# Kernel optimization log

Measured on AMD Instinct MI355X. Metric: run time of the kernel, lower is better.

## Reference

```python
import jax, jax.numpy as jnp
import numpy as np

B, N_UNK, M_KNOWN = 8, 8192, 2048
C1, C2 = 256, 256
MLP = [512, 256, 256]
K_ENC = 32
D = MLP[-1]


def setup_inputs() -> dict:
    key = jax.random.key(0)
    ks = jax.random.split(key, 16)
    return {
        "unknown": jax.random.normal(ks[0], (B, N_UNK, 3), jnp.float32),
        "known": jax.random.normal(ks[1], (B, M_KNOWN, 3), jnp.float32),
        "unknow_feats": jax.random.normal(ks[2], (B, C1, N_UNK), jnp.float32),
        "known_feats": jax.random.normal(ks[3], (B, C2, M_KNOWN), jnp.float32),
        "conv_w1": jax.random.normal(ks[4], (MLP[1], MLP[0]), jnp.float32) * 0.05,
        "conv_b1": jnp.zeros((MLP[1],), jnp.float32),
        "bn_g1": jnp.ones((MLP[1],), jnp.float32),
        "bn_b1": jnp.zeros((MLP[1],), jnp.float32),
        "bn_m1": jax.random.normal(ks[5], (MLP[1],), jnp.float32) * 0.01,
        "bn_v1": jax.random.uniform(ks[6], (MLP[1],), jnp.float32, 0.5, 1.5),
        "conv_w2": jax.random.normal(ks[7], (MLP[2], MLP[1]), jnp.float32) * 0.05,
        "conv_b2": jnp.zeros((MLP[2],), jnp.float32),
        "bn_g2": jnp.ones((MLP[2],), jnp.float32),
        "bn_b2": jnp.zeros((MLP[2],), jnp.float32),
        "bn_m2": jax.random.normal(ks[8], (MLP[2],), jnp.float32) * 0.01,
        "bn_v2": jax.random.uniform(ks[9], (MLP[2],), jnp.float32, 0.5, 1.5),
        "enc_codewords": jax.random.normal(ks[10], (K_ENC, D), jnp.float32) * float(1.0 / np.sqrt(K_ENC * D)),
        "enc_scale": jax.random.uniform(ks[11], (K_ENC,), jnp.float32, -1.0, 0.0),
        "lin_w": jax.random.normal(ks[12], (D, D * K_ENC), jnp.float32) * 0.02,
        "lin_b": jnp.zeros((D,), jnp.float32),
    }


def _conv_bn_relu(x, w, b, g, beta, mean, var):
    # 1x1 conv over (B,C,N) == channel GEMM, then BN (inference form), then ReLU
    x = jnp.einsum("oc,bcn->bon", w, x) + b[None, :, None]
    x = g[None, :, None] * (x - mean[None, :, None]) * jax.lax.rsqrt(var + 1e-5)[None, :, None] + beta[None, :, None]
    return jax.nn.relu(x)


def reference(unknown, known, unknow_feats, known_feats,
              conv_w1, conv_b1, bn_g1, bn_b1, bn_m1, bn_v1,
              conv_w2, conv_b2, bn_g2, bn_b2, bn_m2, bn_v2,
              enc_codewords, enc_scale, lin_w, lin_b):
    # ---- three_nn: 3 nearest known points for each unknown point ----
    x2 = jnp.sum(unknown * unknown, axis=-1)            # (B,n)
    y2 = jnp.sum(known * known, axis=-1)                # (B,m)
    d2 = x2[:, :, None] - 2.0 * jnp.einsum("bnc,bmc->bnm", unknown, known) + y2[:, None, :]
    dist = jnp.sqrt(jnp.maximum(d2, 1e-12))             # (B,n,m) Euclidean
    neg_d, idx = jax.lax.top_k(-dist, 3)                # 3 smallest
    dist3 = -neg_d                                      # (B,n,3)
    dist_recip = 1.0 / (dist3 + 1e-8)
    weight = dist_recip / jnp.sum(dist_recip, axis=2, keepdims=True)
    # ---- three_interpolate: gather + weighted sum ----
    gathered = jax.vmap(lambda f, i: f[:, i])(known_feats, idx)   # (B,C2,n,3)
    interp = jnp.einsum("bcnk,bnk->bcn", gathered, weight)        # (B,C2,n)
    feats = jnp.concatenate([interp, unknow_feats], axis=1)       # (B,C2+C1,n)
    # ---- SharedMLP (two 1x1 conv + BN + ReLU layers) ----
    h = _conv_bn_relu(feats, conv_w1, conv_b1, bn_g1, bn_b1, bn_m1, bn_v1)
    h = _conv_bn_relu(h, conv_w2, conv_b2, bn_g2, bn_b2, bn_m2, bn_v2)   # (B,D,n)
    # ---- Encoding layer (soft dictionary assignment, residual aggregate) ----
    X = jnp.swapaxes(h, 1, 2)                                     # (B,n,D)
    c2 = jnp.sum(enc_codewords * enc_codewords, axis=-1)          # (K,)
    xn2 = jnp.sum(X * X, axis=-1)                                 # (B,n)
    # scaled_l2: s_k * ||x - c_k||^2 without materializing (B,n,K,D) residuals
    sl = enc_scale[None, None, :] * (xn2[:, :, None] - 2.0 * jnp.einsum("bnd,kd->bnk", X, enc_codewords) + c2[None, None, :])
    A = jax.nn.softmax(sl, axis=-1)                               # (B,n,K)
    E = jnp.einsum("bnk,bnd->bkd", A, X) - jnp.sum(A, axis=1)[:, :, None] * enc_codewords[None]
    E = jax.nn.relu(E).reshape(E.shape[0], -1)                    # (B,K*D)
    E = E / jnp.maximum(jnp.linalg.norm(E, axis=1, keepdims=True), 1e-12)  # F.normalize
    ctx = jax.nn.sigmoid(E @ lin_w.T + lin_b)                     # (B,D)
    # ---- channel-attention fusion ----
    return h * ctx[:, :, None]                                    # (B,D,n)
```

## Files before the change

kernel.cpp:

```cpp
#include <hip/hip_runtime.h>
#include <stdint.h>

typedef unsigned short u16;
typedef unsigned int u32;
typedef __attribute__((ext_vector_type(8))) short short8;
typedef __attribute__((ext_vector_type(4))) float f32x4;
typedef __attribute__((ext_vector_type(4))) u32 u32x4;

#define B_ 8
#define N_ 8192
#define M_ 2048
#define DD 256
#define KENC 32

#define SC1 0
#define SH1 256
#define SC2 512
#define SH2 768
#define C2OFF 1024
#define SOFF 1056
#define RNOFF 1088

#define OFF_IDX3   0ull
#define OFF_W3     786432ull
#define OFF_FT     1572864ull
#define OFF_H1T    68681728ull
#define OFF_ERELU  102236160ull
#define OFF_PART   102498304ull
#define OFF_CONSTS 102760448ull
#define OFF_CTX    102768640ull
#define OFF_W1D    102776832ull
#define OFF_W2D    103038976ull
#define OFF_CWD    103170048ull
#define OFF_FLAG   103186432ull

__device__ __forceinline__ float bf2f(u16 v){ return __uint_as_float(((u32)v)<<16); }
__device__ __forceinline__ u16 f2bf(float f){
  u32 x = __float_as_uint(f);
  return (u16)((x + 0x7FFFu + ((x>>16)&1u)) >> 16);
}
__device__ __forceinline__ float ldf(const void* p, size_t i, int f){
  return f ? ((const float*)p)[i] : bf2f(((const u16*)p)[i]);
}

__global__ __launch_bounds__(256) void k_detect(const void* v1, int* flagp){
  __shared__ int cntb, cntf;
  int t = threadIdx.x;
  if (t==0){ cntb=0; cntf=0; }
  __syncthreads();
  float vb = bf2f(((const u16*)v1)[t]);
  if (!(vb > 0.4f && vb < 1.6f)) atomicAdd(&cntb, 1);
  if (t < 64){
    float vf = ((const float*)v1)[t];
    if (!(vf > 0.4f && vf < 1.6f)) atomicAdd(&cntf, 1);
  }
  __syncthreads();
  if (t==0) flagp[0] = (cntb > 0 && cntf == 0) ? 1 : 0;
}

__global__ __launch_bounds__(256) void k_convert(
    const void* w1, const void* w2, const void* cwsrc, const int* __restrict__ flagp,
    u16* __restrict__ W1d, u16* __restrict__ W2d, u16* __restrict__ CWd){
  int id = blockIdx.x*256 + threadIdx.x;
  int f = flagp[0];
  if (id < 131072){
    W1d[id] = f ? f2bf(((const float*)w1)[id]) : ((const u16*)w1)[id];
  } else if (id < 196608){
    int j = id - 131072;
    W2d[j] = f ? f2bf(((const float*)w2)[j]) : ((const u16*)w2)[j];
  } else if (id < 204800){
    int j = id - 196608;
    CWd[j] = f ? f2bf(((const float*)cwsrc)[j]) : ((const u16*)cwsrc)[j];
  }
}

__global__ __launch_bounds__(256) void k0_setup(
    const void* cb1, const void* g1, const void* be1, const void* m1, const void* v1,
    const void* cb2, const void* g2, const void* be2, const void* m2, const void* v2,
    const u16* __restrict__ CWd, const void* es, const int* __restrict__ flagp,
    float* __restrict__ consts){
  int t = threadIdx.x;
  int f = flagp[0];
  {
    float g = ldf(g1,t,f), be = ldf(be1,t,f), m = ldf(m1,t,f), v = ldf(v1,t,f), cb = ldf(cb1,t,f);
    float r = 1.f/sqrtf(v + 1e-5f);
    float sc = g*r;
    consts[SC1+t] = sc; consts[SH1+t] = (cb-m)*sc + be;
  }
  {
    float g = ldf(g2,t,f), be = ldf(be2,t,f), m = ldf(m2,t,f), v = ldf(v2,t,f), cb = ldf(cb2,t,f);
    float r = 1.f/sqrtf(v + 1e-5f);
    float sc = g*r;
    consts[SC2+t] = sc; consts[SH2+t] = (cb-m)*sc + be;
  }
  if (t < KENC){
    float s = 0.f;
    for (int d=0; d<DD; d++){ float c = bf2f(CWd[t*DD+d]); s = fmaf(c,c,s); }
    consts[C2OFF+t] = s;
    consts[SOFF+t]  = ldf(es,t,f);
  }
}

__global__ __launch_bounds__(256) void k1_three_nn(
    const void* unknown, const void* known, const int* __restrict__ flagp,
    int* __restrict__ idx3, float* __restrict__ w3){
  __shared__ float4 kp[M_];
  int b = blockIdx.y, t = threadIdx.x;
  int f = flagp[0];
  for (int i=t; i<M_; i+=256){
    size_t o = ((size_t)b*M_ + i)*3;
    float x = ldf(known,o,f), y = ldf(known,o+1,f), z = ldf(known,o+2,f);
    float y2 = __fadd_rn(__fadd_rn(__fmul_rn(x,x), __fmul_rn(y,y)), __fmul_rn(z,z));
    kp[i] = make_float4(x,y,z,y2);
  }
  __syncthreads();
  int q = t >> 2, sl = t & 3;
  int pid = blockIdx.x*64 + q;
  size_t uo = ((size_t)b*N_ + pid)*3;
  float ux=ldf(unknown,uo,f), uy=ldf(unknown,uo+1,f), uz=ldf(unknown,uo+2,f);
  float x2 = __fadd_rn(__fadd_rn(__fmul_rn(ux,ux), __fmul_rn(uy,uy)), __fmul_rn(uz,uz));
  float b0=3.4e38f, b1=3.4e38f, b2v=3.4e38f;
  int i0=-1, i1=-1, i2=-1;
  int mbase = sl*512;
  for (int mm=0; mm<512; mm+=4){
    float d[4];
    #pragma unroll
    for (int u=0;u<4;u++){
      float4 km = kp[mbase+mm+u];
      float dotv = __fadd_rn(__fadd_rn(__fmul_rn(ux,km.x), __fmul_rn(uy,km.y)), __fmul_rn(uz,km.z));
      d[u] = __fadd_rn(__fsub_rn(x2, __fmul_rn(2.f,dotv)), km.w);
    }
    #pragma unroll
    for (int u=0;u<4;u++){
      float d2 = d[u];
      if (d2 < b2v){
        int m = mbase+mm+u;
        if (d2 < b0){ b2v=b1;i2=i1; b1=b0;i1=i0; b0=d2;i0=m; }
        else if (d2 < b1){ b2v=b1;i2=i1; b1=d2;i1=m; }
        else { b2v=d2; i2=m; }
      }
    }
  }
  #pragma unroll
  for (int delta=1; delta<=2; delta<<=1){
    float o0=__shfl_xor(b0,delta,64), o1=__shfl_xor(b1,delta,64), o2=__shfl_xor(b2v,delta,64);
    int   j0=__shfl_xor(i0,delta,64), j1=__shfl_xor(i1,delta,64), j2=__shfl_xor(i2,delta,64);
    float dv[3] = {o0,o1,o2}; int jv[3] = {j0,j1,j2};
    #pragma unroll
    for (int e=0; e<3; e++){
      float dd = dv[e]; int jj = jv[e];
      bool lt2 = (dd < b2v) || (dd == b2v && jj < i2);
      if (lt2){
        bool lt0 = (dd < b0) || (dd == b0 && jj < i0);
        bool lt1 = (dd < b1) || (dd == b1 && jj < i1);
        if (lt0){ b2v=b1;i2=i1; b1=b0;i1=i0; b0=dd;i0=jj; }
        else if (lt1){ b2v=b1;i2=i1; b1=dd;i1=jj; }
        else { b2v=dd; i2=jj; }
      }
    }
  }
  if (sl == 0){
    float da = __fsqrt_rn(fmaxf(b0,1e-12f));
    float db = __fsqrt_rn(fmaxf(b1,1e-12f));
    float dc = __fsqrt_rn(fmaxf(b2v,1e-12f));
    float r0 = __fdiv_rn(1.f, __fadd_rn(da,1e-8f));
    float r1 = __fdiv_rn(1.f, __fadd_rn(db,1e-8f));
    float r2 = __fdiv_rn(1.f, __fadd_rn(dc,1e-8f));
    float rs = __fadd_rn(__fadd_rn(r0,r1),r2);
    size_t o = ((size_t)b*N_ + pid)*3;
    idx3[o]=i0; idx3[o+1]=i1; idx3[o+2]=i2;
    w3[o]=__fdiv_rn(r0,rs); w3[o+1]=__fdiv_rn(r1,rs); w3[o+2]=__fdiv_rn(r2,rs);
  }
}

__global__ __launch_bounds__(256) void k2_interp(
    const void* kf, const int* __restrict__ idx3,
    const float* __restrict__ w3, const int* __restrict__ flagp, u16* __restrict__ Ft){
  __shared__ u16 Ls[M_*8];
  int ct = blockIdx.x;
  int b = blockIdx.y, t = threadIdx.x;
  int f = flagp[0];
  for (int cp=0; cp<4; cp++){
    int c0 = ct*8 + cp*2;
    size_t base0 = ((size_t)b*DD + c0)*M_;
    size_t base1 = base0 + M_;
    for (int i=t; i<M_; i+=256){
      float f0 = ldf(kf, base0+i, f);
      float f1 = ldf(kf, base1+i, f);
      u32 w = (u32)f2bf(f0) | ((u32)f2bf(f1)<<16);
      *(u32*)(Ls + i*8 + cp*2) = w;
    }
  }
  __syncthreads();
  for (int rep=0; rep<32; rep++){
    int pid = rep*256 + t;
    size_t o3 = ((size_t)b*N_ + pid)*3;
    int ia = idx3[o3], ib = idx3[o3+1], ic = idx3[o3+2];
    float wa = w3[o3], wb = w3[o3+1], wc = w3[o3+2];
    short8 va = *(const short8*)(Ls + ia*8);
    short8 vb = *(const short8*)(Ls + ib*8);
    short8 vc = *(const short8*)(Ls + ic*8);
    u32x4 pk;
    #pragma unroll
    for (int cq=0; cq<4; cq++){
      float fa0 = bf2f((u16)va[cq*2]),   fb0 = bf2f((u16)vb[cq*2]),   fc0 = bf2f((u16)vc[cq*2]);
      float fa1 = bf2f((u16)va[cq*2+1]), fb1 = bf2f((u16)vb[cq*2+1]), fc1 = bf2f((u16)vc[cq*2+1]);
      float v0 = fmaf(wc, fc0, fmaf(wb, fb0, wa*fa0));
      float v1 = fmaf(wc, fc1, fmaf(wb, fb1, wa*fa1));
      pk[cq] = (u32)f2bf(v0) | ((u32)f2bf(v1)<<16);
    }
    *(u32x4*)(Ft + ((size_t)b*N_ + pid)*512 + ct*8) = pk;
  }
}

__global__ __launch_bounds__(256) void k2b_transpose_uf(
    const void* uf, const int* __restrict__ flagp, u16* __restrict__ Ft){
  __shared__ u16 Ls[64*72];
  int bx = blockIdx.x, cy = blockIdx.y, b = blockIdx.z, t = threadIdx.x;
  int f = flagp[0];
  {
    int n = t & 63, cg = t >> 6;
    for (int i=0; i<16; i++){
      int c = cg*16 + i;
      Ls[n*72 + c] = f2bf(ldf(uf, ((size_t)b*DD + cy*64 + c)*N_ + bx*64 + n, f));
    }
  }
  __syncthreads();
  int nl = t>>2, cc = t&3;
  u16* dst = Ft + ((size_t)b*N_ + bx*64 + nl)*512 + 256 + cy*64 + cc*16;
  *(u32x4*)dst     = *(const u32x4*)(Ls + nl*72 + cc*16);
  *(u32x4*)(dst+8) = *(const u32x4*)(Ls + nl*72 + cc*16 + 8);
}

__global__ __launch_bounds__(256) void gemm_bn_relu(
    const u16* __restrict__ W, const u16* __restrict__ Fin,
    const float* __restrict__ consts, int sc_off, int sh_off,
    u16* __restrict__ Out, int K){
  __shared__ u16 SM[17408];
  u16* As = SM; u16* Bs = SM + 4096;
  int b = blockIdx.z, ot = blockIdx.y*128, nt = blockIdx.x*128;
  int t = threadIdx.x, wave = t>>6, lane = t&63, ln = lane&15, quad = lane>>4;
  int wo = (wave&1)*64, wn = (wave>>1)*64;
  f32x4 acc[4][4];
  #pragma unroll
  for (int i=0;i<4;i++)
    #pragma unroll
    for (int j=0;j<4;j++) acc[i][j] = (f32x4)0.f;
  const u16* Wp = W + (size_t)ot*K;
  const u16* Fp = Fin + ((size_t)b*N_ + nt)*K;
  for (int kk=0; kk<K; kk+=32){
    #pragma unroll
    for (int i=0;i<2;i++){
      int ch = t*2 + i;
      int r = ch>>2, kc = (ch&3)*8;
      *(u32x4*)(As + r*32 + kc) = *(const u32x4*)(Wp + (size_t)r*K + kk + kc);
      *(u32x4*)(Bs + r*32 + kc) = *(const u32x4*)(Fp + (size_t)r*K + kk + kc);
    }
    __syncthreads();
    short8 af[4], bfr[4];
    #pragma unroll
    for (int i=0;i<4;i++) af[i]  = *(const short8*)(As + (wo+i*16+ln)*32 + quad*8);
    #pragma unroll
    for (int j=0;j<4;j++) bfr[j] = *(const short8*)(Bs + (wn+j*16+ln)*32 + quad*8);
    #pragma unroll
    for (int i=0;i<4;i++)
      #pragma unroll
      for (int j=0;j<4;j++)
        acc[i][j] = __builtin_amdgcn_mfma_f32_16x16x32_bf16(af[i], bfr[j], acc[i][j], 0,0,0);
    __syncthreads();
  }
  u16* Cs = SM;
  #pragma unroll
  for (int i=0;i<4;i++){
    #pragma unroll
    for (int r=0;r<4;r++){
      int ol = wo + i*16 + quad*4 + r;
      float sc = consts[sc_off + ot + ol], sh = consts[sh_off + ot + ol];
      #pragma unroll
      for (int j=0;j<4;j++){
        float v = fmaxf(fmaf(acc[i][j][r], sc, sh), 0.f);
        Cs[(wn + j*16 + ln)*136 + ol] = f2bf(v);
      }
    }
  }
  __syncthreads();
  int nl = t>>1, half = t&1;
  u16* dst = Out + ((size_t)b*N_ + nt + nl)*256 + ot + half*64;
  const u16* srcr = Cs + nl*136 + half*64;
  #pragma unroll
  for (int c=0;c<8;c++)
    *(u32x4*)(dst + c*8) = *(const u32x4*)(srcr + c*8);
}

__global__ __launch_bounds__(256) void k5_enc_partial(
    const u16* __restrict__ X, const u16* __restrict__ cw,
    const float* __restrict__ consts, float* __restrict__ Epart){
  __shared__ u16 Xs[64*264];
  __shared__ float A_lds[64*32];
  __shared__ float xn2s[64];
  int g = blockIdx.x, b = blockIdx.y, t = threadIdx.x;
  int wave = t>>6, lane = t&63, ln = lane&15, quad = lane>>4;
  int tk = t>>3, tg = t&7;
  float accE[32];
  #pragma unroll
  for (int p=0;p<32;p++) accE[p]=0.f;
  float asum = 0.f;
  float c2v0 = consts[C2OFF + ln], c2v1 = consts[C2OFF + 16 + ln];
  float sv0  = consts[SOFF + ln],  sv1  = consts[SOFF + 16 + ln];
  for (int tt=0; tt<2; tt++){
    int n0 = (g*2+tt)*64;
    const u16* Xp = X + ((size_t)b*N_ + n0)*256;
    #pragma unroll
    for (int i=0;i<8;i++){
      int ch = t + i*256;
      int r = ch>>5, kc = (ch&31)*8;
      *(u32x4*)(Xs + r*264 + kc) = *(const u32x4*)(Xp + r*256 + kc);
    }
    __syncthreads();
    if (t < 64){
      const u16* row = Xs + t*264;
      float s = 0.f;
      for (int d=0; d<256; d+=8){
        short8 xv = *(const short8*)(row + d);
        #pragma unroll
        for (int q=0;q<8;q++){ float x = bf2f((u16)xv[q]); s = fmaf(x,x,s); }
      }
      xn2s[t] = s;
    }
    __syncthreads();
    f32x4 pj0 = (f32x4)0.f, pj1 = (f32x4)0.f;
    const u16* xrow = Xs + (wave*16 + ln)*264;
    #pragma unroll
    for (int kk=0; kk<256; kk+=32){
      short8 a   = *(const short8*)(xrow + kk + quad*8);
      short8 bf0 = *(const short8*)(cw + (size_t)ln*256 + kk + quad*8);
      short8 bf1 = *(const short8*)(cw + (size_t)(16+ln)*256 + kk + quad*8);
      pj0 = __builtin_amdgcn_mfma_f32_16x16x32_bf16(a, bf0, pj0, 0,0,0);
      pj1 = __builtin_amdgcn_mfma_f32_16x16x32_bf16(a, bf1, pj1, 0,0,0);
    }
    #pragma unroll
    for (int r=0;r<4;r++){
      int nl = wave*16 + quad*4 + r;
      float xv = xn2s[nl];
      float v0 = sv0 * __fadd_rn(__fsub_rn(xv, __fmul_rn(2.f,pj0[r])), c2v0);
      float v1 = sv1 * __fadd_rn(__fsub_rn(xv, __fmul_rn(2.f,pj1[r])), c2v1);
      float mx = fmaxf(v0,v1);
      #pragma unroll
      for (int d=1; d<16; d<<=1) mx = fmaxf(mx, __shfl_xor(mx, d, 64));
      float e0 = __expf(v0-mx), e1 = __expf(v1-mx);
      float es = e0+e1;
      #pragma unroll
      for (int d=1; d<16; d<<=1) es += __shfl_xor(es, d, 64);
      float inv = 1.f/es;
      A_lds[nl*32 + ln]      = e0*inv;
      A_lds[nl*32 + 16 + ln] = e1*inv;
    }
    __syncthreads();
    #pragma unroll 2
    for (int n=0; n<64; n++){
      float a = A_lds[n*32 + tk];
      asum += a;
      const u16* xr = Xs + n*264 + tg*32;
      #pragma unroll
      for (int p8=0; p8<4; p8++){
        u32x4 xv = *(const u32x4*)(xr + p8*8);
        #pragma unroll
        for (int q=0; q<4; q++){
          u32 w = xv[q];
          float lo = __uint_as_float(w<<16);
          float hi = __uint_as_float(w & 0xffff0000u);
          accE[p8*8 + q*2]   = fmaf(a, lo, accE[p8*8 + q*2]);
          accE[p8*8 + q*2+1] = fmaf(a, hi, accE[p8*8 + q*2+1]);
        }
      }
    }
    __syncthreads();
  }
  int slab = b*64 + g;
  float* Ed = Epart + (size_t)slab*8224 + (size_t)tk*257;
  #pragma unroll
  for (int p=0;p<32;p++) Ed[tg*32 + p] = accE[p];
  if (tg==0) Ed[256] = asum;
}

__global__ __launch_bounds__(256) void k5b_reduce(
    const float* __restrict__ Epart, const u16* __restrict__ cw, float* __restrict__ Erelu){
  int id = blockIdx.x*256 + threadIdx.x;
  int d = id & 255, k = (id>>8)&31, b = id>>13;
  float s = 0.f, as = 0.f;
  for (int sl=0; sl<64; sl++){
    const float* Ep = Epart + ((size_t)(b*64+sl))*8224 + (size_t)k*257;
    s  += Ep[d];
    as += Ep[256];
  }
  float cv = bf2f(cw[k*256+d]);
  Erelu[(size_t)b*8192 + k*256 + d] = fmaxf(s - as*cv, 0.f);
}

__global__ __launch_bounds__(256) void k6a_norm(
    const float* __restrict__ Erelu, float* __restrict__ consts){
  __shared__ float red[256];
  int b = blockIdx.x, t = threadIdx.x;
  float s = 0.f;
  for (int i=0;i<32;i++){ float e = Erelu[(size_t)b*8192 + i*256 + t]; s = fmaf(e,e,s); }
  red[t] = s; __syncthreads();
  for (int w=128; w>0; w>>=1){ if (t<w) red[t] += red[t+w]; __syncthreads(); }
  if (t==0) consts[RNOFF + b] = 1.f/fmaxf(__fsqrt_rn(red[0]), 1e-12f);
}

__global__ __launch_bounds__(256) void k6b_partial(
    const float* __restrict__ Erelu, const void* lw, const int* __restrict__ flagp,
    float* __restrict__ partials){
  __shared__ float Er[256];
  int kc = blockIdx.x, b = blockIdx.y, t = threadIdx.x;
  int f = flagp[0];
  Er[t] = Erelu[(size_t)b*8192 + kc*256 + t];
  __syncthreads();
  float s = 0.f;
  if (f){
    const float* lwp = (const float*)lw + (size_t)t*8192 + kc*256;
    for (int p=0; p<256; p+=4){
      f32x4 v = *(const f32x4*)(lwp + p);
      #pragma unroll
      for (int q=0;q<4;q++) s = fmaf(Er[p+q], v[q], s);
    }
  } else {
    const u16* lwp = (const u16*)lw + (size_t)t*8192 + kc*256;
    for (int p=0; p<256; p+=8){
      u32x4 v = *(const u32x4*)(lwp + p);
      #pragma unroll
      for (int q=0;q<4;q++){
        u32 w = v[q];
        s = fmaf(Er[p+q*2],   __uint_as_float(w<<16), s);
        s = fmaf(Er[p+q*2+1], __uint_as_float(w & 0xffff0000u), s);
      }
    }
  }
  partials[((size_t)b*32 + kc)*256 + t] = s;
}

__global__ __launch_bounds__(256) void k6c_ctx(
    const float* __restrict__ partials, const float* __restrict__ consts,
    const void* lb, const int* __restrict__ flagp, float* __restrict__ ctx){
  int b = blockIdx.x, t = threadIdx.x;
  int f = flagp[0];
  float s = 0.f;
  for (int kc=0; kc<32; kc++) s += partials[((size_t)b*32+kc)*256 + t];
  float x = fmaf(consts[RNOFF+b], s, ldf(lb,t,f));
  ctx[b*256 + t] = 1.f/(1.f + __expf(-x));
}

__global__ __launch_bounds__(256) void k7_out(
    const u16* __restrict__ ht, const float* __restrict__ ctx,
    const int* __restrict__ flagp, void* out){
  __shared__ u16 Ls[64*72];
  int bx = blockIdx.x, oy = blockIdx.y, b = blockIdx.z, t = threadIdx.x;
  int f = flagp[0];
  {
    int nl = t>>2, oc = t&3;
    const u16* src = ht + ((size_t)b*N_ + bx*64 + nl)*256 + oy*64 + oc*16;
    *(u32x4*)(Ls + nl*72 + oc*16)     = *(const u32x4*)src;
    *(u32x4*)(Ls + nl*72 + oc*16 + 8) = *(const u32x4*)(src + 8);
  }
  __syncthreads();
  int ol = t>>2, nc = t&3;
  float cv = ctx[b*256 + oy*64 + ol];
  size_t dstoff = ((size_t)b*DD + oy*64 + ol)*N_ + bx*64 + nc*16;
  if (f){
    float* dst = (float*)out + dstoff;
    #pragma unroll
    for (int wq=0; wq<4; wq++){
      f32x4 v;
      #pragma unroll
      for (int q=0;q<4;q++) v[q] = bf2f(Ls[(nc*16 + wq*4 + q)*72 + ol]) * cv;
      *(f32x4*)(dst + wq*4) = v;
    }
  } else {
    u32 words[8];
    #pragma unroll
    for (int wq=0; wq<8; wq++){
      float v0 = bf2f(Ls[(nc*16 + wq*2)*72 + ol]) * cv;
      float v1 = bf2f(Ls[(nc*16 + wq*2+1)*72 + ol]) * cv;
      words[wq] = (u32)f2bf(v0) | ((u32)f2bf(v1)<<16);
    }
    u16* dst = (u16*)out + dstoff;
    u32x4 w0 = {words[0],words[1],words[2],words[3]};
    u32x4 w1 = {words[4],words[5],words[6],words[7]};
    *(u32x4*)dst     = w0;
    *(u32x4*)(dst+8) = w1;
  }
}

extern "C" void kernel_launch(void* const* d_in, const int* in_sizes, int n_in,
                              void* d_out, int out_size, void* d_ws, size_t ws_size,
                              hipStream_t stream){
  const void* unknown = d_in[0];
  const void* known   = d_in[1];
  const void* uf      = d_in[2];
  const void* kf      = d_in[3];
  const void* w1      = d_in[4];
  const void* cb1     = d_in[5];
  const void* g1      = d_in[6];
  const void* be1     = d_in[7];
  const void* m1      = d_in[8];
  const void* v1      = d_in[9];
  const void* w2      = d_in[10];
  const void* cb2     = d_in[11];
  const void* g2      = d_in[12];
  const void* be2     = d_in[13];
  const void* m2      = d_in[14];
  const void* v2      = d_in[15];
  const void* cw      = d_in[16];
  const void* es      = d_in[17];
  const void* lw      = d_in[18];
  const void* lb      = d_in[19];

  char* ws = (char*)d_ws;
  int*   idx3  = (int*)(ws + OFF_IDX3);
  float* w3    = (float*)(ws + OFF_W3);
  u16*   Ft    = (u16*)(ws + OFF_FT);
  u16*   ht    = Ft;
  u16*   h1t   = (u16*)(ws + OFF_H1T);
  float* Epart = (float*)(ws + OFF_H1T);
  float* Erelu    = (float*)(ws + OFF_ERELU);
  float* partials = (float*)(ws + OFF_PART);
  float* consts   = (float*)(ws + OFF_CONSTS);
  float* ctx      = (float*)(ws + OFF_CTX);
  u16*   W1d   = (u16*)(ws + OFF_W1D);
  u16*   W2d   = (u16*)(ws + OFF_W2D);
  u16*   CWd   = (u16*)(ws + OFF_CWD);
  int*   flagp = (int*)(ws + OFF_FLAG);

  k_detect<<<1, 256, 0, stream>>>(v1, flagp);
  k_convert<<<800, 256, 0, stream>>>(w1, w2, cw, flagp, W1d, W2d, CWd);
  k0_setup<<<1, 256, 0, stream>>>(cb1,g1,be1,m1,v1, cb2,g2,be2,m2,v2, CWd, es, flagp, consts);
  k1_three_nn<<<dim3(128,8), 256, 0, stream>>>(unknown, known, flagp, idx3, w3);
  k2_interp<<<dim3(32,8), 256, 0, stream>>>(kf, idx3, w3, flagp, Ft);
  k2b_transpose_uf<<<dim3(128,4,8), 256, 0, stream>>>(uf, flagp, Ft);
  gemm_bn_relu<<<dim3(64,2,8), 256, 0, stream>>>(W1d, Ft,  consts, SC1, SH1, h1t, 512);
  gemm_bn_relu<<<dim3(64,2,8), 256, 0, stream>>>(W2d, h1t, consts, SC2, SH2, ht,  256);
  k5_enc_partial<<<dim3(64,8), 256, 0, stream>>>(ht, CWd, consts, Epart);
  k5b_reduce<<<256, 256, 0, stream>>>(Epart, CWd, Erelu);
  k6a_norm<<<8, 256, 0, stream>>>(Erelu, consts);
  k6b_partial<<<dim3(32,8), 256, 0, stream>>>(Erelu, lw, flagp, partials);
  k6c_ctx<<<8, 256, 0, stream>>>(partials, consts, lb, flagp, ctx);
  k7_out<<<dim3(128,4,8), 256, 0, stream>>>(ht, ctx, flagp, d_out);
}
```

Measured before the change: 480.9 us.

## Process two queries per thread in three_nn and split interp over row groups

The three_nn kernel now has each thread handle two unknown points, so every shared-memory load of a known point feeds two distance computations, and the grid is halved. Each lane's slice of known points is interleaved rather than contiguous, which changes the LDS access pattern. The interpolation kernel is split over 4 row groups per batch, giving 4x more blocks (256 to 1024) for better occupancy, at the cost of each block reloading its known-feature tile into shared memory.

Measured after the change: 512.7 us. 1.07x slower.

```diff
diff --git a/kernel.cpp b/kernel.cpp
--- a/kernel.cpp
+++ b/kernel.cpp
@@ -114,62 +114,72 @@
     kp[i] = make_float4(x,y,z,y2);
   }
   __syncthreads();
-  int q = t >> 2, sl = t & 3;
-  int pid = blockIdx.x*64 + q;
-  size_t uo = ((size_t)b*N_ + pid)*3;
-  float ux=ldf(unknown,uo,f), uy=ldf(unknown,uo+1,f), uz=ldf(unknown,uo+2,f);
-  float x2 = __fadd_rn(__fadd_rn(__fmul_rn(ux,ux), __fmul_rn(uy,uy)), __fmul_rn(uz,uz));
-  float b0=3.4e38f, b1=3.4e38f, b2v=3.4e38f;
-  int i0=-1, i1=-1, i2=-1;
-  int mbase = sl*512;
-  for (int mm=0; mm<512; mm+=4){
-    float d[4];
-    #pragma unroll
-    for (int u=0;u<4;u++){
-      float4 km = kp[mbase+mm+u];
-      float dotv = __fadd_rn(__fadd_rn(__fmul_rn(ux,km.x), __fmul_rn(uy,km.y)), __fmul_rn(uz,km.z));
-      d[u] = __fadd_rn(__fsub_rn(x2, __fmul_rn(2.f,dotv)), km.w);
-    }
-    #pragma unroll
-    for (int u=0;u<4;u++){
-      float d2 = d[u];
-      if (d2 < b2v){
-        int m = mbase+mm+u;
-        if (d2 < b0){ b2v=b1;i2=i1; b1=b0;i1=i0; b0=d2;i0=m; }
-        else if (d2 < b1){ b2v=b1;i2=i1; b1=d2;i1=m; }
-        else { b2v=d2; i2=m; }
+  int qq = t >> 2, sl = t & 3;
+  int pid0 = blockIdx.x*128 + qq;
+  int pid1 = pid0 + 64;
+  float ux[2], uy[2], uz[2], x2[2];
+  #pragma unroll
+  for (int qi=0; qi<2; qi++){
+    size_t uo = ((size_t)b*N_ + (qi ? pid1 : pid0))*3;
+    ux[qi]=ldf(unknown,uo,f); uy[qi]=ldf(unknown,uo+1,f); uz[qi]=ldf(unknown,uo+2,f);
+    x2[qi] = __fadd_rn(__fadd_rn(__fmul_rn(ux[qi],ux[qi]), __fmul_rn(uy[qi],uy[qi])), __fmul_rn(uz[qi],uz[qi]));
+  }
+  float b0[2], b1[2], b2v[2];
+  int i0[2], i1[2], i2[2];
+  #pragma unroll
+  for (int qi=0; qi<2; qi++){ b0[qi]=3.4e38f; b1[qi]=3.4e38f; b2v[qi]=3.4e38f; i0[qi]=-1; i1[qi]=-1; i2[qi]=-1; }
+  for (int mm=0; mm<128; mm++){
+    #pragma unroll
+    for (int u=0; u<4; u++){
+      int m = mm*16 + u*4 + sl;
+      float4 km = kp[m];
+      #pragma unroll
+      for (int qi=0; qi<2; qi++){
+        float dotv = __fadd_rn(__fadd_rn(__fmul_rn(ux[qi],km.x), __fmul_rn(uy[qi],km.y)), __fmul_rn(uz[qi],km.z));
+        float d2 = __fadd_rn(__fsub_rn(x2[qi], __fmul_rn(2.f,dotv)), km.w);
+        if (d2 < b2v[qi]){
+          if (d2 < b0[qi]){ b2v[qi]=b1[qi];i2[qi]=i1[qi]; b1[qi]=b0[qi];i1[qi]=i0[qi]; b0[qi]=d2;i0[qi]=m; }
+          else if (d2 < b1[qi]){ b2v[qi]=b1[qi];i2[qi]=i1[qi]; b1[qi]=d2;i1[qi]=m; }
+          else { b2v[qi]=d2; i2[qi]=m; }
+        }
       }
     }
   }
   #pragma unroll
   for (int delta=1; delta<=2; delta<<=1){
-    float o0=__shfl_xor(b0,delta,64), o1=__shfl_xor(b1,delta,64), o2=__shfl_xor(b2v,delta,64);
-    int   j0=__shfl_xor(i0,delta,64), j1=__shfl_xor(i1,delta,64), j2=__shfl_xor(i2,delta,64);
-    float dv[3] = {o0,o1,o2}; int jv[3] = {j0,j1,j2};
-    #pragma unroll
-    for (int e=0; e<3; e++){
-      float dd = dv[e]; int jj = jv[e];
-      bool lt2 = (dd < b2v) || (dd == b2v && jj < i2);
-      if (lt2){
-        bool lt0 = (dd < b0) || (dd == b0 && jj < i0);
-        bool lt1 = (dd < b1) || (dd == b1 && jj < i1);
-        if (lt0){ b2v=b1;i2=i1; b1=b0;i1=i0; b0=dd;i0=jj; }
-        else if (lt1){ b2v=b1;i2=i1; b1=dd;i1=jj; }
-        else { b2v=dd; i2=jj; }
+    #pragma unroll
+    for (int qi=0; qi<2; qi++){
+      float o0=__shfl_xor(b0[qi],delta,64), o1=__shfl_xor(b1[qi],delta,64), o2=__shfl_xor(b2v[qi],delta,64);
+      int   j0=__shfl_xor(i0[qi],delta,64), j1=__shfl_xor(i1[qi],delta,64), j2=__shfl_xor(i2[qi],delta,64);
+      float dv[3] = {o0,o1,o2}; int jv[3] = {j0,j1,j2};
+      #pragma unroll
+      for (int e=0; e<3; e++){
+        float dd = dv[e]; int jj = jv[e];
+        bool lt2 = (dd < b2v[qi]) || (dd == b2v[qi] && jj < i2[qi]);
+        if (lt2){
+          bool lt0 = (dd < b0[qi]) || (dd == b0[qi] && jj < i0[qi]);
+          bool lt1 = (dd < b1[qi]) || (dd == b1[qi] && jj < i1[qi]);
+          if (lt0){ b2v[qi]=b1[qi];i2[qi]=i1[qi]; b1[qi]=b0[qi];i1[qi]=i0[qi]; b0[qi]=dd;i0[qi]=jj; }
+          else if (lt1){ b2v[qi]=b1[qi];i2[qi]=i1[qi]; b1[qi]=dd;i1[qi]=jj; }
+          else { b2v[qi]=dd; i2[qi]=jj; }
+        }
       }
     }
   }
   if (sl == 0){
-    float da = __fsqrt_rn(fmaxf(b0,1e-12f));
-    float db = __fsqrt_rn(fmaxf(b1,1e-12f));
-    float dc = __fsqrt_rn(fmaxf(b2v,1e-12f));
-    float r0 = __fdiv_rn(1.f, __fadd_rn(da,1e-8f));
-    float r1 = __fdiv_rn(1.f, __fadd_rn(db,1e-8f));
-    float r2 = __fdiv_rn(1.f, __fadd_rn(dc,1e-8f));
-    float rs = __fadd_rn(__fadd_rn(r0,r1),r2);
-    size_t o = ((size_t)b*N_ + pid)*3;
-    idx3[o]=i0; idx3[o+1]=i1; idx3[o+2]=i2;
-    w3[o]=__fdiv_rn(r0,rs); w3[o+1]=__fdiv_rn(r1,rs); w3[o+2]=__fdiv_rn(r2,rs);
+    #pragma unroll
+    for (int qi=0; qi<2; qi++){
+      float da = __fsqrt_rn(fmaxf(b0[qi],1e-12f));
+      float db = __fsqrt_rn(fmaxf(b1[qi],1e-12f));
+      float dc = __fsqrt_rn(fmaxf(b2v[qi],1e-12f));
+      float r0 = __fdiv_rn(1.f, __fadd_rn(da,1e-8f));
+      float r1 = __fdiv_rn(1.f, __fadd_rn(db,1e-8f));
+      float r2 = __fdiv_rn(1.f, __fadd_rn(dc,1e-8f));
+      float rs = __fadd_rn(__fadd_rn(r0,r1),r2);
+      size_t o = ((size_t)b*N_ + (qi ? pid1 : pid0))*3;
+      idx3[o]=i0[qi]; idx3[o+1]=i1[qi]; idx3[o+2]=i2[qi];
+      w3[o]=__fdiv_rn(r0,rs); w3[o+1]=__fdiv_rn(r1,rs); w3[o+2]=__fdiv_rn(r2,rs);
+    }
   }
 }
 
@@ -178,7 +188,8 @@
     const float* __restrict__ w3, const int* __restrict__ flagp, u16* __restrict__ Ft){
   __shared__ u16 Ls[M_*8];
   int ct = blockIdx.x;
-  int b = blockIdx.y, t = threadIdx.x;
+  int rg = blockIdx.y;
+  int b = blockIdx.z, t = threadIdx.x;
   int f = flagp[0];
   for (int cp=0; cp<4; cp++){
     int c0 = ct*8 + cp*2;
@@ -192,7 +203,7 @@
     }
   }
   __syncthreads();
-  for (int rep=0; rep<32; rep++){
+  for (int rep=rg*8; rep<rg*8+8; rep++){
     int pid = rep*256 + t;
     size_t o3 = ((size_t)b*N_ + pid)*3;
     int ia = idx3[o3], ib = idx3[o3+1], ic = idx3[o3+2];
@@ -534,8 +545,8 @@
   k_detect<<<1, 256, 0, stream>>>(v1, flagp);
   k_convert<<<800, 256, 0, stream>>>(w1, w2, cw, flagp, W1d, W2d, CWd);
   k0_setup<<<1, 256, 0, stream>>>(cb1,g1,be1,m1,v1, cb2,g2,be2,m2,v2, CWd, es, flagp, consts);
-  k1_three_nn<<<dim3(128,8), 256, 0, stream>>>(unknown, known, flagp, idx3, w3);
-  k2_interp<<<dim3(32,8), 256, 0, stream>>>(kf, idx3, w3, flagp, Ft);
+  k1_three_nn<<<dim3(64,8), 256, 0, stream>>>(unknown, known, flagp, idx3, w3);
+  k2_interp<<<dim3(32,4,8), 256, 0, stream>>>(kf, idx3, w3, flagp, Ft);
   k2b_transpose_uf<<<dim3(128,4,8), 256, 0, stream>>>(uf, flagp, Ft);
   gemm_bn_relu<<<dim3(64,2,8), 256, 0, stream>>>(W1d, Ft,  consts, SC1, SH1, h1t, 512);
   gemm_bn_relu<<<dim3(64,2,8), 256, 0, stream>>>(W2d, h1t, consts, SC2, SH2, ht,  256);
```
